# Kernel optimization log

Hardware: AMD Instinct MI355X
Metric: run time of the kernel (lower is better)

The kernel has to match this reference:

```python
import jax, jax.numpy as jnp
import numpy as np

B, NS, NF, D, H = 64, 16, 4096, 128, 256  # batch, n_slots, n_feat, slot_dim, mlp_hidden
EPS_LN = 1e-5
EPS_ATT = 1e-8


def _layernorm(x, g, b):
    mu = x.mean(-1, keepdims=True)
    var = x.var(-1, keepdims=True)
    return (x - mu) / jnp.sqrt(var + EPS_LN) * g + b


def setup_inputs() -> dict:
    key = jax.random.key(0)
    ks = jax.random.split(key, 8)
    s = 0.02  # init scale for weights
    return {
        "t": jnp.zeros((), jnp.float32),
        "slots": jax.random.normal(ks[0], (B, NS, D), jnp.float32),
        "k": jax.random.normal(ks[1], (B, NF, D), jnp.float32),
        "v": jax.random.normal(ks[2], (B, NF, D), jnp.float32),
        "Wq": jax.random.normal(ks[3], (D, D), jnp.float32) * s,           # eqx Linear weight [out,in], no bias
        "ln_slots_g": jnp.ones((D,), jnp.float32),
        "ln_slots_b": jnp.zeros((D,), jnp.float32),
        "W_ih": jax.random.normal(ks[4], (3 * D, D), jnp.float32) * s,     # GRUCell input weights
        "W_hh": jax.random.normal(ks[5], (3 * D, D), jnp.float32) * s,     # GRUCell hidden weights
        "b_ih": jnp.zeros((3 * D,), jnp.float32),
        "b_n": jnp.zeros((D,), jnp.float32),
        "ln_ff_g": jnp.ones((D,), jnp.float32),
        "ln_ff_b": jnp.zeros((D,), jnp.float32),
        "W0": jax.random.normal(ks[6], (H, D), jnp.float32) * s,
        "b0": jnp.zeros((H,), jnp.float32),
        "W1": jax.random.normal(ks[7], (D, H), jnp.float32) * s,
        "b1": jnp.zeros((D,), jnp.float32),
    }


def reference(t, slots, k, v, Wq, ln_slots_g, ln_slots_b,
              W_ih, W_hh, b_ih, b_n, ln_ff_g, ln_ff_b, W0, b0, W1, b1):
    scale = D ** (-0.5)
    # LayerNorm over slot features, then query projection
    slots_norm = _layernorm(slots, ln_slots_g, ln_slots_b)
    q = jnp.einsum('bnd,ed->bne', slots_norm, Wq)                    # [B,NS,D]
    # Doubly-normalized slot attention: softmax over slots (axis=1), renorm over features
    att_logits = jnp.einsum('bnd,bmd->bnm', q, k) * scale            # [B,NS,NF]
    att = jax.nn.softmax(att_logits, axis=1)
    att = att / (att.sum(axis=-1, keepdims=True) + EPS_ATT)
    attended = jnp.einsum('bnm,bmd->bnd', att, v)                    # [B,NS,D]
    # GRUCell (equinox semantics): gates order (reset, input, new)
    igates = jnp.einsum('bnd,ed->bne', attended, W_ih) + b_ih        # [B,NS,3D]
    hgates = jnp.einsum('bnd,ed->bne', slots, W_hh)                  # [B,NS,3D]
    ir, ii, inew = jnp.split(igates, 3, axis=-1)
    hr, hi, hnew = jnp.split(hgates, 3, axis=-1)
    reset = jax.nn.sigmoid(ir + hr)
    inp = jax.nn.sigmoid(ii + hi)
    new = jnp.tanh(inew + reset * (hnew + b_n))
    gru_out = new + inp * (slots - new)                              # [B,NS,D]
    # LayerNorm -> MLP residual
    gru_normed = _layernorm(gru_out, ln_ff_g, ln_ff_b)
    h = jax.nn.relu(jnp.einsum('bnd,hd->bnh', gru_normed, W0) + b0)
    h = jnp.einsum('bnh,dh->bnd', h, W1) + b1
    target = gru_out + h
    return target - slots
```

## Files before the change

kernel.cpp:

```cpp
#include <hip/hip_runtime.h>
#include <hip/hip_bf16.h>
#include <math.h>

#define B_  64
#define NS_ 16
#define NF_ 4096
#define D_  128
#define H_  256


typedef __attribute__((ext_vector_type(8))) short bf16x8;
typedef __attribute__((ext_vector_type(4))) float f32x4;

__device__ __forceinline__ bf16x8 as_bf16x8(uint4 u) {
    union { uint4 u; bf16x8 h; } c; c.u = u; return c.h;
}

__device__ __forceinline__ unsigned int pk_bf16(float a, float b) {
    unsigned int ua = __float_as_uint(a), ub = __float_as_uint(b);
    ua = (ua + 0x7FFFu + ((ua >> 16) & 1u)) >> 16;
    ub = (ub + 0x7FFFu + ((ub >> 16) & 1u)) >> 16;
    return ua | (ub << 16);
}

__device__ __forceinline__ float dot4(float4 a, float4 b) {
    return a.x * b.x + a.y * b.y + a.z * b.z + a.w * b.w;
}

__global__ __launch_bounds__(128) void k_q(
    const float* __restrict__ slots, const float* __restrict__ Wq,
    const float* __restrict__ lng, const float* __restrict__ lnb,
    unsigned int* __restrict__ q_out, float* __restrict__ acc, float* __restrict__ den) {
    const int b = blockIdx.x;
    const int t = threadIdx.x;
    __shared__ float sl_s[16][128];
    __shared__ float norm_s[16][128];
    __shared__ float st_s[16][8][2];
    __shared__ float mu_s[16], rs_s[16];
    __shared__ float q_s[16][128];

    const float4* sp = (const float4*)(slots + (size_t)b * 2048);
#pragma unroll
    for (int i = 0; i < 4; ++i) {
        int f = i * 128 + t;
        *(float4*)&sl_s[f >> 5][(f & 31) * 4] = sp[f];
    }
    __syncthreads();

    {
        int n = t >> 3, j = t & 7;
        float s1 = 0.f, s2 = 0.f;
#pragma unroll
        for (int d2 = 0; d2 < 16; ++d2) {
            float x = sl_s[n][j * 16 + d2];
            s1 += x; s2 += x * x;
        }
        st_s[n][j][0] = s1; st_s[n][j][1] = s2;
    }
    __syncthreads();
    if (t < 16) {
        float s1 = 0.f, s2 = 0.f;
#pragma unroll
        for (int j = 0; j < 8; ++j) { s1 += st_s[t][j][0]; s2 += st_s[t][j][1]; }
        float mu = s1 * (1.0f / 128.0f);
        float var = s2 * (1.0f / 128.0f) - mu * mu;
        mu_s[t] = mu;
        rs_s[t] = rsqrtf(var + 1e-5f);
    }
    __syncthreads();

    float gl = lng[t], bl = lnb[t];
#pragma unroll
    for (int n = 0; n < 16; ++n)
        norm_s[n][t] = (sl_s[n][t] - mu_s[n]) * rs_s[n] * gl + bl;
    __syncthreads();

    const float4* wq = (const float4*)(Wq + (size_t)t * 128);
    float qn[16];
#pragma unroll
    for (int n = 0; n < 16; ++n) qn[n] = 0.f;
#pragma unroll 4
    for (int j = 0; j < 32; ++j) {
        float4 w4 = wq[j];
#pragma unroll
        for (int n = 0; n < 16; ++n) qn[n] += dot4(w4, *(const float4*)&norm_s[n][4 * j]);
    }
#pragma unroll
    for (int n = 0; n < 16; ++n) q_s[n][t] = qn[n];

    float4 z4 = make_float4(0.f, 0.f, 0.f, 0.f);
    float4* ab = (float4*)(acc + (size_t)b * 2048);
#pragma unroll
    for (int i = 0; i < 4; ++i) ab[i * 128 + t] = z4;
    if (t < 16) den[b * 16 + t] = 0.f;
    __syncthreads();

    unsigned int* qo = q_out + (size_t)b * 1024;
#pragma unroll
    for (int i = 0; i < 8; ++i) {
        int u = i * 128 + t;
        int n = u >> 6, e2 = u & 63;
        qo[n * 64 + e2] = pk_bf16(q_s[n][2 * e2], q_s[n][2 * e2 + 1]);
    }
}

__global__ __launch_bounds__(256) void k_attn(
    const float* __restrict__ kg_, const float* __restrict__ vg_,
    const unsigned int* __restrict__ q_u, float* __restrict__ acc_g, float* __restrict__ denom_g) {
    const int t = threadIdx.x;
    const int w = t >> 6, l = t & 63;
    const int b = blockIdx.y;
    const int lm = l & 15;
    const int g  = l >> 4;
    const int dcol = t & 127;
    const int nh = t >> 7;

    __shared__ unsigned int lds_u[5632];
    unsigned int* k_s = lds_u;
    float*        p_s = (float*)(lds_u + 4352);

    uint4 qA[4];
    {
        const uint4* qb = (const uint4*)q_u + ((b * 16 + lm) * 16);
#pragma unroll
        for (int kk = 0; kk < 4; ++kk) qA[kk] = qb[kk * 4 + g];
    }

    float acc[16];
#pragma unroll
    for (int i = 0; i < 16; ++i) acc[i] = 0.f;
    float dn[4] = {0.f, 0.f, 0.f, 0.f};

    const size_t mbase = (size_t)b * NF_ + blockIdx.x * 128;
    const float4* kg4 = (const float4*)kg_ + (mbase + w * 16) * 32;
    const float*  vgp = vg_ + mbase * 128 + dcol;

    for (int sub = 0; sub < 2; ++sub) {
        const float* vt = vgp + (size_t)(sub * 64 + nh * 32) * 128;

        const float4* kp = kg4 + sub * 64 * 32;
        float4 ka[4], kb4[4];
#pragma unroll
        for (int i = 0; i < 4; ++i) ka[i] = kp[i * 64 + l];
#pragma unroll
        for (int i = 0; i < 4; ++i) kb4[i] = kp[(4 + i) * 64 + l];

        float vva[8], vvb[8];
#pragma unroll
        for (int i = 0; i < 8; ++i) vva[i] = vt[i * 128];
#pragma unroll
        for (int i = 0; i < 8; ++i) vvb[i] = vt[(8 + i) * 128];

#pragma unroll
        for (int i = 0; i < 4; ++i) {
            int r = w * 16 + 2 * i + (l >> 5);
            *(uint2*)&k_s[r * 68 + 2 * (l & 31)] =
                make_uint2(pk_bf16(ka[i].x, ka[i].y), pk_bf16(ka[i].z, ka[i].w));
        }
#pragma unroll
        for (int i = 0; i < 4; ++i) {
            int r = w * 16 + 2 * (4 + i) + (l >> 5);
            *(uint2*)&k_s[r * 68 + 2 * (l & 31)] =
                make_uint2(pk_bf16(kb4[i].x, kb4[i].y), pk_bf16(kb4[i].z, kb4[i].w));
        }

        f32x4 sacc = {0.f, 0.f, 0.f, 0.f};
#pragma unroll
        for (int kk = 0; kk < 4; ++kk) {
            uint4 kf = *(const uint4*)&k_s[(w * 16 + lm) * 68 + kk * 16 + g * 4];
            sacc = __builtin_amdgcn_mfma_f32_16x16x32_bf16(
                as_bf16x8(qA[kk]), as_bf16x8(kf), sacc, 0, 0, 0);
        }
        const float scale = 0.08838834764831845f;
        float e0 = __expf(sacc[0] * scale);
        float e1 = __expf(sacc[1] * scale);
        float e2 = __expf(sacc[2] * scale);
        float e3 = __expf(sacc[3] * scale);
        float se = (e0 + e1) + (e2 + e3);
        se += __shfl_xor(se, 16);
        se += __shfl_xor(se, 32);
        float rse = __builtin_amdgcn_rcpf(se);
        float4 pv4 = make_float4(e0 * rse, e1 * rse, e2 * rse, e3 * rse);
        dn[0] += pv4.x; dn[1] += pv4.y; dn[2] += pv4.z; dn[3] += pv4.w;
        *(float4*)&p_s[(w * 16 + lm) * 20 + g * 4] = pv4;
        __syncthreads();

#define PV_CONSUME(VREG, BASE)                                              \
        {                                                                   \
            _Pragma("unroll")                                               \
            for (int i = 0; i < 8; ++i) {                                   \
                int m = nh * 32 + (BASE) + i;                               \
                float vvi = VREG[i];                                        \
                float4 pa = *(const float4*)&p_s[m * 20 + 0];               \
                float4 pb = *(const float4*)&p_s[m * 20 + 4];               \
                float4 pc = *(const float4*)&p_s[m * 20 + 8];               \
                float4 pd = *(const float4*)&p_s[m * 20 + 12];              \
                acc[0]  = fmaf(pa.x, vvi, acc[0]);                          \
                acc[1]  = fmaf(pa.y, vvi, acc[1]);                          \
                acc[2]  = fmaf(pa.z, vvi, acc[2]);                          \
                acc[3]  = fmaf(pa.w, vvi, acc[3]);                          \
                acc[4]  = fmaf(pb.x, vvi, acc[4]);                          \
                acc[5]  = fmaf(pb.y, vvi, acc[5]);                          \
                acc[6]  = fmaf(pb.z, vvi, acc[6]);                          \
                acc[7]  = fmaf(pb.w, vvi, acc[7]);                          \
                acc[8]  = fmaf(pc.x, vvi, acc[8]);                          \
                acc[9]  = fmaf(pc.y, vvi, acc[9]);                          \
                acc[10] = fmaf(pc.z, vvi, acc[10]);                         \
                acc[11] = fmaf(pc.w, vvi, acc[11]);                         \
                acc[12] = fmaf(pd.x, vvi, acc[12]);                         \
                acc[13] = fmaf(pd.y, vvi, acc[13]);                         \
                acc[14] = fmaf(pd.z, vvi, acc[14]);                         \
                acc[15] = fmaf(pd.w, vvi, acc[15]);                         \
            }                                                               \
        }
        PV_CONSUME(vva, 0)
#pragma unroll
        for (int i = 0; i < 8; ++i) vva[i] = vt[(16 + i) * 128];
        PV_CONSUME(vvb, 8)
#pragma unroll
        for (int i = 0; i < 8; ++i) vvb[i] = vt[(24 + i) * 128];
        PV_CONSUME(vva, 16)
        PV_CONSUME(vvb, 24)
#undef PV_CONSUME
        __syncthreads();
    }

#pragma unroll
    for (int m = 1; m <= 8; m <<= 1) {
#pragma unroll
        for (int r = 0; r < 4; ++r) dn[r] += __shfl_xor(dn[r], m);
    }
    if (lm == 0) {
#pragma unroll
        for (int r = 0; r < 4; ++r)
            atomicAdd(denom_g + b * 16 + g * 4 + r, dn[r]);
    }
    float* red = (float*)lds_u;
    if (nh == 1) {
#pragma unroll
        for (int i = 0; i < 4; ++i)
            *(float4*)&red[dcol * 16 + 4 * i] = *(const float4*)&acc[4 * i];
    }
    __syncthreads();
    if (nh == 0) {
        float* base = acc_g + (size_t)b * 2048 + dcol;
#pragma unroll
        for (int n = 0; n < 16; ++n)
            atomicAdd(base + n * 128, acc[n] + red[dcol * 16 + n]);
    }
}

__global__ __launch_bounds__(256) void k_final(
    const float* __restrict__ acc_g, const float* __restrict__ denom_g,
    const float* __restrict__ slots,
    const float* __restrict__ W_ih, const float* __restrict__ W_hh,
    const float* __restrict__ b_ih, const float* __restrict__ b_n,
    const float* __restrict__ ffg, const float* __restrict__ ffb,
    const float* __restrict__ W0, const float* __restrict__ b0,
    const float* __restrict__ W1, const float* __restrict__ b1,
    float* __restrict__ out) {
    const int bn0 = blockIdx.x * 4;
    const int t = threadIdx.x;
    __shared__ float att_s[4][128], slot_s[4][128];
    __shared__ float gates_s[4][4][128];
    __shared__ float gru_s[4][128], gn_s[4][128];
    __shared__ float h_s[4][256];

#pragma unroll
    for (int idx = t; idx < 512; idx += 256) {
        int bi = idx >> 7, d = idx & 127;
        int bn = bn0 + bi;
        float den = denom_g[bn] + 1e-8f;
        att_s[bi][d] = acc_g[(size_t)bn * 128 + d] / den;
        slot_s[bi][d] = slots[(size_t)bn * 128 + d];
    }
    __syncthreads();

    for (int g = t; g < 384; g += 256) {
        const float4* wi = (const float4*)(W_ih + (size_t)g * 128);
        const float4* wh = (const float4*)(W_hh + (size_t)g * 128);
        float si[4] = {0.f, 0.f, 0.f, 0.f}, sh[4] = {0.f, 0.f, 0.f, 0.f};
#pragma unroll 4
        for (int j = 0; j < 32; ++j) {
            float4 wi4 = wi[j], wh4 = wh[j];
#pragma unroll
            for (int bi = 0; bi < 4; ++bi) {
                si[bi] += dot4(wi4, *(const float4*)&att_s[bi][4 * j]);
                sh[bi] += dot4(wh4, *(const float4*)&slot_s[bi][4 * j]);
            }
        }
        float bih = b_ih[g];
        int d = g & 127;
#pragma unroll
        for (int bi = 0; bi < 4; ++bi) {
            if (g < 128)       gates_s[bi][0][d] = si[bi] + sh[bi] + bih;
            else if (g < 256)  gates_s[bi][1][d] = si[bi] + sh[bi] + bih;
            else { gates_s[bi][2][d] = si[bi] + bih; gates_s[bi][3][d] = sh[bi]; }
        }
    }
    __syncthreads();

    {
        int bi = t >> 6, l = t & 63;
        float gr[2], s1 = 0.f, s2 = 0.f;
#pragma unroll
        for (int h = 0; h < 2; ++h) {
            int d = l + 64 * h;
            float rr = 1.f / (1.f + __expf(-gates_s[bi][0][d]));
            float ii = 1.f / (1.f + __expf(-gates_s[bi][1][d]));
            float nv = tanhf(gates_s[bi][2][d] + rr * (gates_s[bi][3][d] + b_n[d]));
            float gru = nv + ii * (slot_s[bi][d] - nv);
            gr[h] = gru;
            gru_s[bi][d] = gru;
            s1 += gru; s2 += gru * gru;
        }
#pragma unroll
        for (int m = 1; m < 64; m <<= 1) { s1 += __shfl_xor(s1, m); s2 += __shfl_xor(s2, m); }
        float mu = s1 * (1.0f / 128.0f);
        float var = s2 * (1.0f / 128.0f) - mu * mu;
        float rstd = rsqrtf(var + 1e-5f);
#pragma unroll
        for (int h = 0; h < 2; ++h) {
            int d = l + 64 * h;
            gn_s[bi][d] = (gr[h] - mu) * rstd * ffg[d] + ffb[d];
        }
    }
    __syncthreads();

    {
        const float4* w0 = (const float4*)(W0 + (size_t)t * 128);
        float s[4] = {0.f, 0.f, 0.f, 0.f};
#pragma unroll 4
        for (int j = 0; j < 32; ++j) {
            float4 w4 = w0[j];
#pragma unroll
            for (int bi = 0; bi < 4; ++bi) s[bi] += dot4(w4, *(const float4*)&gn_s[bi][4 * j]);
        }
        float b0v = b0[t];
#pragma unroll
        for (int bi = 0; bi < 4; ++bi) h_s[bi][t] = fmaxf(s[bi] + b0v, 0.f);
    }
    __syncthreads();

    {
        int dr = t & 127, bp = (t >> 7) * 2;
        const float4* w1 = (const float4*)(W1 + (size_t)dr * 256);
        float s[2] = {0.f, 0.f};
#pragma unroll 4
        for (int j = 0; j < 64; ++j) {
            float4 w4 = w1[j];
#pragma unroll
            for (int u = 0; u < 2; ++u) s[u] += dot4(w4, *(const float4*)&h_s[bp + u][4 * j]);
        }
        float b1v = b1[dr];
#pragma unroll
        for (int u = 0; u < 2; ++u) {
            int bi = bp + u;
            out[(size_t)(bn0 + bi) * 128 + dr] = gru_s[bi][dr] + s[u] + b1v - slot_s[bi][dr];
        }
    }
}

extern "C" void kernel_launch(void* const* d_in, const int* in_sizes, int n_in,
                              void* d_out, int out_size, void* d_ws, size_t ws_size,
                              hipStream_t stream) {
    const float* slots = (const float*)d_in[1];
    const float* k     = (const float*)d_in[2];
    const float* v     = (const float*)d_in[3];
    const float* Wq    = (const float*)d_in[4];
    const float* lng   = (const float*)d_in[5];
    const float* lnb   = (const float*)d_in[6];
    const float* W_ih  = (const float*)d_in[7];
    const float* W_hh  = (const float*)d_in[8];
    const float* b_ih  = (const float*)d_in[9];
    const float* b_n   = (const float*)d_in[10];
    const float* ffg   = (const float*)d_in[11];
    const float* ffb   = (const float*)d_in[12];
    const float* W0    = (const float*)d_in[13];
    const float* b0    = (const float*)d_in[14];
    const float* W1    = (const float*)d_in[15];
    const float* b1    = (const float*)d_in[16];

    char* ws = (char*)d_ws;
    unsigned int* q_u = (unsigned int*)ws;
    float* acc = (float*)(ws + 262144);
    float* den = (float*)(ws + 786432);

    k_q<<<dim3(B_), dim3(128), 0, stream>>>(slots, Wq, lng, lnb, q_u, acc, den);
    k_attn<<<dim3(32, B_), dim3(256), 0, stream>>>(k, v, q_u, acc, den);
    k_final<<<dim3(256), dim3(256), 0, stream>>>(acc, den, slots, W_ih, W_hh,
                                                 b_ih, b_n, ffg, ffb, W0, b0, W1, b1,
                                                 (float*)d_out);
}
```

Baseline: 375.8 us.

## Split query and final kernels into more blocks, pad attention reduction LDS

```diff
diff --git a/kernel.cpp b/kernel.cpp
--- a/kernel.cpp
+++ b/kernel.cpp
@@ -31,73 +31,60 @@
     const float* __restrict__ slots, const float* __restrict__ Wq,
     const float* __restrict__ lng, const float* __restrict__ lnb,
     unsigned int* __restrict__ q_out, float* __restrict__ acc, float* __restrict__ den) {
-    const int b = blockIdx.x;
+    const int bid = blockIdx.x;
+    const int b = bid >> 2, q4 = bid & 3;
     const int t = threadIdx.x;
-    __shared__ float sl_s[16][128];
-    __shared__ float norm_s[16][128];
-    __shared__ float st_s[16][8][2];
-    __shared__ float mu_s[16], rs_s[16];
-    __shared__ float q_s[16][128];
-
-    const float4* sp = (const float4*)(slots + (size_t)b * 2048);
-#pragma unroll
-    for (int i = 0; i < 4; ++i) {
-        int f = i * 128 + t;
-        *(float4*)&sl_s[f >> 5][(f & 31) * 4] = sp[f];
-    }
-    __syncthreads();
-
-    {
-        int n = t >> 3, j = t & 7;
-        float s1 = 0.f, s2 = 0.f;
-#pragma unroll
-        for (int d2 = 0; d2 < 16; ++d2) {
-            float x = sl_s[n][j * 16 + d2];
-            s1 += x; s2 += x * x;
-        }
-        st_s[n][j][0] = s1; st_s[n][j][1] = s2;
-    }
-    __syncthreads();
-    if (t < 16) {
-        float s1 = 0.f, s2 = 0.f;
-#pragma unroll
-        for (int j = 0; j < 8; ++j) { s1 += st_s[t][j][0]; s2 += st_s[t][j][1]; }
+    const int w = t >> 6, l = t & 63;
+    __shared__ float norm_s[4][128];
+    __shared__ float st_s[4][2][2];
+    __shared__ float q_s[4][128];
+
+    float sl[4];
+#pragma unroll
+    for (int r = 0; r < 4; ++r)
+        sl[r] = slots[(size_t)b * 2048 + (q4 * 4 + r) * 128 + t];
+
+#pragma unroll
+    for (int r = 0; r < 4; ++r) {
+        float s1 = sl[r], s2 = sl[r] * sl[r];
+#pragma unroll
+        for (int m = 1; m < 64; m <<= 1) { s1 += __shfl_xor(s1, m); s2 += __shfl_xor(s2, m); }
+        if (l == 0) { st_s[r][w][0] = s1; st_s[r][w][1] = s2; }
+    }
+    __syncthreads();
+
+    float gl = lng[t], bl = lnb[t];
+#pragma unroll
+    for (int r = 0; r < 4; ++r) {
+        float s1 = st_s[r][0][0] + st_s[r][1][0];
+        float s2 = st_s[r][0][1] + st_s[r][1][1];
         float mu = s1 * (1.0f / 128.0f);
         float var = s2 * (1.0f / 128.0f) - mu * mu;
-        mu_s[t] = mu;
-        rs_s[t] = rsqrtf(var + 1e-5f);
-    }
-    __syncthreads();
-
-    float gl = lng[t], bl = lnb[t];
-#pragma unroll
-    for (int n = 0; n < 16; ++n)
-        norm_s[n][t] = (sl_s[n][t] - mu_s[n]) * rs_s[n] * gl + bl;
+        float rs = rsqrtf(var + 1e-5f);
+        norm_s[r][t] = (sl[r] - mu) * rs * gl + bl;
+    }
     __syncthreads();
 
     const float4* wq = (const float4*)(Wq + (size_t)t * 128);
-    float qn[16];
-#pragma unroll
-    for (int n = 0; n < 16; ++n) qn[n] = 0.f;
+    float qn[4] = {0.f, 0.f, 0.f, 0.f};
 #pragma unroll 4
     for (int j = 0; j < 32; ++j) {
         float4 w4 = wq[j];
 #pragma unroll
-        for (int n = 0; n < 16; ++n) qn[n] += dot4(w4, *(const float4*)&norm_s[n][4 * j]);
-    }
-#pragma unroll
-    for (int n = 0; n < 16; ++n) q_s[n][t] = qn[n];
-
-    float4 z4 = make_float4(0.f, 0.f, 0.f, 0.f);
-    float4* ab = (float4*)(acc + (size_t)b * 2048);
-#pragma unroll
-    for (int i = 0; i < 4; ++i) ab[i * 128 + t] = z4;
-    if (t < 16) den[b * 16 + t] = 0.f;
-    __syncthreads();
-
-    unsigned int* qo = q_out + (size_t)b * 1024;
-#pragma unroll
-    for (int i = 0; i < 8; ++i) {
+        for (int r = 0; r < 4; ++r) qn[r] += dot4(w4, *(const float4*)&norm_s[r][4 * j]);
+    }
+#pragma unroll
+    for (int r = 0; r < 4; ++r) q_s[r][t] = qn[r];
+
+#pragma unroll
+    for (int r = 0; r < 4; ++r)
+        acc[(size_t)b * 2048 + (q4 * 4 + r) * 128 + t] = 0.f;
+    if (t < 4) den[b * 16 + q4 * 4 + t] = 0.f;
+    __syncthreads();
+
+    unsigned int* qo = q_out + (size_t)b * 1024 + q4 * 256;
+#pragma unroll
+    for (int i = 0; i < 2; ++i) {
         int u = i * 128 + t;
         int n = u >> 6, e2 = u & 63;
         qo[n * 64 + e2] = pk_bf16(q_s[n][2 * e2], q_s[n][2 * e2 + 1]);
@@ -238,15 +225,14 @@
     float* red = (float*)lds_u;
     if (nh == 1) {
 #pragma unroll
-        for (int i = 0; i < 4; ++i)
-            *(float4*)&red[dcol * 16 + 4 * i] = *(const float4*)&acc[4 * i];
+        for (int n = 0; n < 16; ++n) red[dcol * 17 + n] = acc[n];
     }
     __syncthreads();
     if (nh == 0) {
         float* base = acc_g + (size_t)b * 2048 + dcol;
 #pragma unroll
         for (int n = 0; n < 16; ++n)
-            atomicAdd(base + n * 128, acc[n] + red[dcol * 16 + n]);
+            atomicAdd(base + n * 128, acc[n] + red[dcol * 17 + n]);
     }
 }
 
@@ -259,105 +245,83 @@
     const float* __restrict__ W0, const float* __restrict__ b0,
     const float* __restrict__ W1, const float* __restrict__ b1,
     float* __restrict__ out) {
-    const int bn0 = blockIdx.x * 4;
+    const int bn = blockIdx.x;
     const int t = threadIdx.x;
-    __shared__ float att_s[4][128], slot_s[4][128];
-    __shared__ float gates_s[4][4][128];
-    __shared__ float gru_s[4][128], gn_s[4][128];
-    __shared__ float h_s[4][256];
-
-#pragma unroll
-    for (int idx = t; idx < 512; idx += 256) {
-        int bi = idx >> 7, d = idx & 127;
-        int bn = bn0 + bi;
+    __shared__ float att_s[128], slot_s[128];
+    __shared__ float gates_s[4][128];
+    __shared__ float gru_s[128], gn_s[128];
+    __shared__ float h_s[256];
+    __shared__ float stat_s[2];
+    __shared__ float red2[128];
+
+    if (t < 128) {
         float den = denom_g[bn] + 1e-8f;
-        att_s[bi][d] = acc_g[(size_t)bn * 128 + d] / den;
-        slot_s[bi][d] = slots[(size_t)bn * 128 + d];
+        att_s[t] = acc_g[(size_t)bn * 128 + t] / den;
+    } else {
+        slot_s[t - 128] = slots[(size_t)bn * 128 + (t - 128)];
     }
     __syncthreads();
 
     for (int g = t; g < 384; g += 256) {
         const float4* wi = (const float4*)(W_ih + (size_t)g * 128);
         const float4* wh = (const float4*)(W_hh + (size_t)g * 128);
-        float si[4] = {0.f, 0.f, 0.f, 0.f}, sh[4] = {0.f, 0.f, 0.f, 0.f};
+        float si = 0.f, sh = 0.f;
 #pragma unroll 4
         for (int j = 0; j < 32; ++j) {
-            float4 wi4 = wi[j], wh4 = wh[j];
-#pragma unroll
-            for (int bi = 0; bi < 4; ++bi) {
-                si[bi] += dot4(wi4, *(const float4*)&att_s[bi][4 * j]);
-                sh[bi] += dot4(wh4, *(const float4*)&slot_s[bi][4 * j]);
-            }
+            si += dot4(wi[j], *(const float4*)&att_s[4 * j]);
+            sh += dot4(wh[j], *(const float4*)&slot_s[4 * j]);
         }
         float bih = b_ih[g];
-        int d = g & 127;
-#pragma unroll
-        for (int bi = 0; bi < 4; ++bi) {
-            if (g < 128)       gates_s[bi][0][d] = si[bi] + sh[bi] + bih;
-            else if (g < 256)  gates_s[bi][1][d] = si[bi] + sh[bi] + bih;
-            else { gates_s[bi][2][d] = si[bi] + bih; gates_s[bi][3][d] = sh[bi]; }
-        }
-    }
-    __syncthreads();
-
-    {
-        int bi = t >> 6, l = t & 63;
-        float gr[2], s1 = 0.f, s2 = 0.f;
-#pragma unroll
-        for (int h = 0; h < 2; ++h) {
-            int d = l + 64 * h;
-            float rr = 1.f / (1.f + __expf(-gates_s[bi][0][d]));
-            float ii = 1.f / (1.f + __expf(-gates_s[bi][1][d]));
-            float nv = tanhf(gates_s[bi][2][d] + rr * (gates_s[bi][3][d] + b_n[d]));
-            float gru = nv + ii * (slot_s[bi][d] - nv);
-            gr[h] = gru;
-            gru_s[bi][d] = gru;
-            s1 += gru; s2 += gru * gru;
-        }
+        if (g < 128)      gates_s[0][g] = si + sh + bih;
+        else if (g < 256) gates_s[1][g - 128] = si + sh + bih;
+        else { gates_s[2][g - 256] = si + bih; gates_s[3][g - 256] = sh; }
+    }
+    __syncthreads();
+
+    if (t < 128) {
+        float rr = 1.f / (1.f + __expf(-gates_s[0][t]));
+        float ii = 1.f / (1.f + __expf(-gates_s[1][t]));
+        float nv = tanhf(gates_s[2][t] + rr * (gates_s[3][t] + b_n[t]));
+        gru_s[t] = nv + ii * (slot_s[t] - nv);
+    }
+    __syncthreads();
+
+    if (t < 64) {
+        float a = gru_s[t], c = gru_s[t + 64];
+        float s1 = a + c, s2 = a * a + c * c;
 #pragma unroll
         for (int m = 1; m < 64; m <<= 1) { s1 += __shfl_xor(s1, m); s2 += __shfl_xor(s2, m); }
-        float mu = s1 * (1.0f / 128.0f);
-        float var = s2 * (1.0f / 128.0f) - mu * mu;
-        float rstd = rsqrtf(var + 1e-5f);
-#pragma unroll
-        for (int h = 0; h < 2; ++h) {
-            int d = l + 64 * h;
-            gn_s[bi][d] = (gr[h] - mu) * rstd * ffg[d] + ffb[d];
-        }
-    }
+        if (t == 0) {
+            float mu = s1 * (1.0f / 128.0f);
+            float var = s2 * (1.0f / 128.0f) - mu * mu;
+            stat_s[0] = mu;
+            stat_s[1] = rsqrtf(var + 1e-5f);
+        }
+    }
+    __syncthreads();
+    if (t < 128)
+        gn_s[t] = (gru_s[t] - stat_s[0]) * stat_s[1] * ffg[t] + ffb[t];
     __syncthreads();
 
     {
         const float4* w0 = (const float4*)(W0 + (size_t)t * 128);
-        float s[4] = {0.f, 0.f, 0.f, 0.f};
+        float s = 0.f;
 #pragma unroll 4
-        for (int j = 0; j < 32; ++j) {
-            float4 w4 = w0[j];
-#pragma unroll
-            for (int bi = 0; bi < 4; ++bi) s[bi] += dot4(w4, *(const float4*)&gn_s[bi][4 * j]);
-        }
-        float b0v = b0[t];
-#pragma unroll
-        for (int bi = 0; bi < 4; ++bi) h_s[bi][t] = fmaxf(s[bi] + b0v, 0.f);
+        for (int j = 0; j < 32; ++j) s += dot4(w0[j], *(const float4*)&gn_s[4 * j]);
+        h_s[t] = fmaxf(s + b0[t], 0.f);
     }
     __syncthreads();
 
     {
-        int dr = t & 127, bp = (t >> 7) * 2;
-        const float4* w1 = (const float4*)(W1 + (size_t)dr * 256);
-        float s[2] = {0.f, 0.f};
+        int d = t & 127, half = t >> 7;
+        const float4* w1 = (const float4*)(W1 + (size_t)d * 256 + half * 128);
+        float s = 0.f;
 #pragma unroll 4
-        for (int j = 0; j < 64; ++j) {
-            float4 w4 = w1[j];
-#pragma unroll
-            for (int u = 0; u < 2; ++u) s[u] += dot4(w4, *(const float4*)&h_s[bp + u][4 * j]);
-        }
-        float b1v = b1[dr];
-#pragma unroll
-        for (int u = 0; u < 2; ++u) {
-            int bi = bp + u;
-            out[(size_t)(bn0 + bi) * 128 + dr] = gru_s[bi][dr] + s[u] + b1v - slot_s[bi][dr];
-        }
+        for (int j = 0; j < 32; ++j) s += dot4(w1[j], *(const float4*)&h_s[half * 128 + 4 * j]);
+        if (half == 1) red2[d] = s;
+        __syncthreads();
+        if (half == 0)
+            out[(size_t)bn * 128 + d] = gru_s[d] + s + red2[d] + b1[d] - slot_s[d];
     }
 }
 
@@ -386,9 +350,9 @@
     float* acc = (float*)(ws + 262144);
     float* den = (float*)(ws + 786432);
 
-    k_q<<<dim3(B_), dim3(128), 0, stream>>>(slots, Wq, lng, lnb, q_u, acc, den);
+    k_q<<<dim3(256), dim3(128), 0, stream>>>(slots, Wq, lng, lnb, q_u, acc, den);
     k_attn<<<dim3(32, B_), dim3(256), 0, stream>>>(k, v, q_u, acc, den);
-    k_final<<<dim3(256), dim3(256), 0, stream>>>(acc, den, slots, W_ih, W_hh,
-                                                 b_ih, b_n, ffg, ffb, W0, b0, W1, b1,
-                                                 (float*)d_out);
-}
+    k_final<<<dim3(1024), dim3(256), 0, stream>>>(acc, den, slots, W_ih, W_hh,
+                                                  b_ih, b_n, ffg, ffb, W0, b0, W1, b1,
+                                                  (float*)d_out);
+}
```

After: 401.3 us. 6.8% more time.

## Double per-block feature chunk and replace atomic accumulation with partial-sum buffer

Applied to the files above, without the earlier changes.

```diff
diff --git a/kernel.cpp b/kernel.cpp
--- a/kernel.cpp
+++ b/kernel.cpp
@@ -104,9 +104,11 @@
     }
 }
 
+template<int PART>
 __global__ __launch_bounds__(256) void k_attn(
     const float* __restrict__ kg_, const float* __restrict__ vg_,
-    const unsigned int* __restrict__ q_u, float* __restrict__ acc_g, float* __restrict__ denom_g) {
+    const unsigned int* __restrict__ q_u, float* __restrict__ acc_g,
+    float* __restrict__ part, float* __restrict__ denom_g) {
     const int t = threadIdx.x;
     const int w = t >> 6, l = t & 63;
     const int b = blockIdx.y;
@@ -131,11 +133,11 @@
     for (int i = 0; i < 16; ++i) acc[i] = 0.f;
     float dn[4] = {0.f, 0.f, 0.f, 0.f};
 
-    const size_t mbase = (size_t)b * NF_ + blockIdx.x * 128;
+    const size_t mbase = (size_t)b * NF_ + blockIdx.x * 256;
     const float4* kg4 = (const float4*)kg_ + (mbase + w * 16) * 32;
     const float*  vgp = vg_ + mbase * 128 + dcol;
 
-    for (int sub = 0; sub < 2; ++sub) {
+    for (int sub = 0; sub < 4; ++sub) {
         const float* vt = vgp + (size_t)(sub * 64 + nh * 32) * 128;
 
         const float4* kp = kg4 + sub * 64 * 32;
@@ -238,21 +240,28 @@
     float* red = (float*)lds_u;
     if (nh == 1) {
 #pragma unroll
-        for (int i = 0; i < 4; ++i)
-            *(float4*)&red[dcol * 16 + 4 * i] = *(const float4*)&acc[4 * i];
+        for (int n = 0; n < 16; ++n) red[dcol * 17 + n] = acc[n];
     }
     __syncthreads();
     if (nh == 0) {
-        float* base = acc_g + (size_t)b * 2048 + dcol;
-#pragma unroll
-        for (int n = 0; n < 16; ++n)
-            atomicAdd(base + n * 128, acc[n] + red[dcol * 16 + n]);
-    }
-}
-
+        if (PART) {
+            float* base = part + ((size_t)(b * 16 + blockIdx.x) * 16) * 128 + dcol;
+#pragma unroll
+            for (int n = 0; n < 16; ++n)
+                base[n * 128] = acc[n] + red[dcol * 17 + n];
+        } else {
+            float* base = acc_g + (size_t)b * 2048 + dcol;
+#pragma unroll
+            for (int n = 0; n < 16; ++n)
+                atomicAdd(base + n * 128, acc[n] + red[dcol * 17 + n]);
+        }
+    }
+}
+
+template<int PART>
 __global__ __launch_bounds__(256) void k_final(
-    const float* __restrict__ acc_g, const float* __restrict__ denom_g,
-    const float* __restrict__ slots,
+    const float* __restrict__ acc_g, const float* __restrict__ part,
+    const float* __restrict__ denom_g, const float* __restrict__ slots,
     const float* __restrict__ W_ih, const float* __restrict__ W_hh,
     const float* __restrict__ b_ih, const float* __restrict__ b_n,
     const float* __restrict__ ffg, const float* __restrict__ ffb,
@@ -271,7 +280,16 @@
         int bi = idx >> 7, d = idx & 127;
         int bn = bn0 + bi;
         float den = denom_g[bn] + 1e-8f;
-        att_s[bi][d] = acc_g[(size_t)bn * 128 + d] / den;
+        float s;
+        if (PART) {
+            const float* pp = part + ((size_t)(bn >> 4) * 256 + (bn & 15)) * 128 + d;
+            s = 0.f;
+#pragma unroll
+            for (int c = 0; c < 16; ++c) s += pp[c * 2048];
+        } else {
+            s = acc_g[(size_t)bn * 128 + d];
+        }
+        att_s[bi][d] = s / den;
         slot_s[bi][d] = slots[(size_t)bn * 128 + d];
     }
     __syncthreads();
@@ -383,12 +401,22 @@
 
     char* ws = (char*)d_ws;
     unsigned int* q_u = (unsigned int*)ws;
-    float* acc = (float*)(ws + 262144);
-    float* den = (float*)(ws + 786432);
+    float* acc  = (float*)(ws + 262144);
+    float* den  = (float*)(ws + 786432);
+    float* partp = (float*)(ws + 1048576);
+
+    const bool use_part = (ws_size >= (size_t)1048576 + 64u * 16u * 16u * 128u * 4u);
 
     k_q<<<dim3(B_), dim3(128), 0, stream>>>(slots, Wq, lng, lnb, q_u, acc, den);
-    k_attn<<<dim3(32, B_), dim3(256), 0, stream>>>(k, v, q_u, acc, den);
-    k_final<<<dim3(256), dim3(256), 0, stream>>>(acc, den, slots, W_ih, W_hh,
-                                                 b_ih, b_n, ffg, ffb, W0, b0, W1, b1,
-                                                 (float*)d_out);
-}
+    if (use_part) {
+        k_attn<1><<<dim3(16, B_), dim3(256), 0, stream>>>(k, v, q_u, acc, partp, den);
+        k_final<1><<<dim3(256), dim3(256), 0, stream>>>(acc, partp, den, slots,
+                                                        W_ih, W_hh, b_ih, b_n, ffg, ffb,
+                                                        W0, b0, W1, b1, (float*)d_out);
+    } else {
+        k_attn<0><<<dim3(16, B_), dim3(256), 0, stream>>>(k, v, q_u, acc, partp, den);
+        k_final<0><<<dim3(256), dim3(256), 0, stream>>>(acc, partp, den, slots,
+                                                        W_ih, W_hh, b_ih, b_n, ffg, ffb,
+                                                        W0, b0, W1, b1, (float*)d_out);
+    }
+}
```

Measured after the change: 368.6 us. No clear change (-1.9%).
